# Kernel tuning notes

Measured on AMD Instinct MI355X. Metric: run time of the kernel, lower is better.

## Reference

```python
import jax, jax.numpy as jnp
import numpy as np

N_NODES = 100000
N_EDGES = 1600000
S_FEAT = 16   # static node features
D_FEAT = 8    # dynamic node features
E_FEAT = 4    # edge features
K = 2
EDGE_IN = E_FEAT + 2 * S_FEAT + 2 * D_FEAT  # 52
HIDDEN = 2 * D_FEAT                          # 16


def setup_inputs() -> dict:
    key = jax.random.key(0)
    ks = jax.random.split(key, 12)
    inp = {
        "x_s": jax.random.normal(ks[0], (N_NODES, S_FEAT), jnp.float32),
        "x_d": jax.random.normal(ks[1], (N_NODES, D_FEAT), jnp.float32),
        "edge_attr": jax.random.normal(ks[2], (N_EDGES, E_FEAT), jnp.float32),
        # edge MLP: Linear(EDGE_IN->HIDDEN) + ReLU + Linear(HIDDEN->D_FEAT)
        "W1": jax.random.normal(ks[3], (HIDDEN, EDGE_IN), jnp.float32) / np.sqrt(EDGE_IN),
        "b1": jnp.zeros((HIDDEN,), jnp.float32),
        "W2": jax.random.normal(ks[4], (D_FEAT, HIDDEN), jnp.float32) / np.sqrt(HIDDEN),
        "b2": jnp.zeros((D_FEAT,), jnp.float32),
        # K+1 = 3 filter matrices, Linear(D->D, bias=False): y = x @ W.T
        "Wf0": jax.random.normal(ks[5], (D_FEAT, D_FEAT), jnp.float32) / np.sqrt(D_FEAT),
        "Wf1": jax.random.normal(ks[6], (D_FEAT, D_FEAT), jnp.float32) / np.sqrt(D_FEAT),
        "Wf2": jax.random.normal(ks[7], (D_FEAT, D_FEAT), jnp.float32) / np.sqrt(D_FEAT),
        "edge_index": jax.random.randint(ks[8], (2, N_EDGES), 0, N_NODES, jnp.int64
                                         if jax.config.jax_enable_x64 else jnp.int32),
    }
    return inp


def _edge_mlp(e, W1, b1, W2, b2):
    h = jax.nn.relu(e @ W1.T + b1)
    return h @ W2.T + b2


def reference(x_s, x_d, edge_attr, W1, b1, W2, b2, Wf0, Wf1, Wf2, edge_index):
    row, col = edge_index[0], edge_index[1]
    num_nodes = x_d.shape[0]

    # s_ij depends only on static inputs (x_s, x_d, edge_attr), not on `out`,
    # so it is identical across the K steps; compute it once. The per-step
    # boolean edge mask is applied multiplicatively below, which matches the
    # torch masked-gather/scatter exactly (normalization is per-edge).
    e_ij = jnp.concatenate(
        [x_s[row], x_s[col], x_d[row], x_d[col], edge_attr], axis=1)  # [E, 52]
    s_ij = _edge_mlp(e_ij, W1, b1, W2, b2)                            # [E, D]
    nrm = jnp.linalg.norm(s_ij, axis=1, keepdims=True)
    s_ij = jnp.where(nrm > 0, s_ij / jnp.where(nrm > 0, nrm, 1.0), 0.0)

    filters = [Wf0, Wf1, Wf2]
    out = x_d @ filters[0].T
    for k in range(K):
        mask = out.sum(1) != 0                         # [N]
        edge_mask = (mask[row] | mask[col]).astype(out.dtype)  # [E]
        hydraulic_gradient = out[col] - out[row]       # [E, D]
        shift_sum = hydraulic_gradient * s_ij * edge_mask[:, None]
        scattered = jax.ops.segment_sum(shift_sum, col, num_segments=num_nodes)
        scattered = scattered @ filters[k + 1].T
        out = out + scattered
    return out
```

## Files before the change

### kernel.cpp

```cpp
#include <hip/hip_runtime.h>
#include <hip/hip_fp16.h>

#define S_FEAT 16
#define D_FEAT 8
#define E_FEAT 4
#define EDGE_IN 52
#define HIDDEN 16
#define SCAN_CHUNK 2048
#define NSUB 8

typedef unsigned int uint4v __attribute__((ext_vector_type(4)));
typedef float float4v __attribute__((ext_vector_type(4)));

__device__ __forceinline__ uint4v pack_rec(const float s[8], int row)
{
    int q[8];
#pragma unroll
    for (int i = 0; i < 8; ++i) {
        float v = fminf(fmaxf(s[i] * 2047.f, -2047.f), 2047.f);
        q[i] = (int)rintf(v) & 0xFFF;
    }
    uint4v r;
    r[0] = (unsigned)(q[0] | (q[1] << 12) | (q[2] << 24));
    r[1] = (unsigned)((q[2] >> 8) | (q[3] << 4) | (q[4] << 16) | (q[5] << 28));
    r[2] = (unsigned)((q[5] >> 4) | (q[6] << 8) | (q[7] << 20));
    r[3] = (unsigned)row;
    return r;
}

__device__ __forceinline__ float rec_s(uint4v r, int f)
{
    int off = f * 12;
    unsigned lo = off < 32 ? r[0] : (off < 64 ? r[1] : r[2]);
    unsigned hi = off < 32 ? r[1] : (off < 64 ? r[2] : 0u);
    unsigned sh = (unsigned)off & 31u;
    unsigned long long both = ((unsigned long long)hi << 32) | lo;
    int q = ((int)((unsigned)(both >> sh) << 20)) >> 20;
    return (float)q * (1.f / 2047.f);
}

__device__ __forceinline__ void unpack8h(uint4v w, float* dst)
{
#pragma unroll
    for (int i = 0; i < 4; ++i) {
        unsigned u = w[i];
        __half2 h = *reinterpret_cast<__half2*>(&u);
        float2 f = __half22float2(h);
        dst[2 * i] = f.x; dst[2 * i + 1] = f.y;
    }
}

__device__ __forceinline__ void proj_node(
    int n, const float* __restrict__ x_s, const float* __restrict__ x_d,
    const float* __restrict__ W1, const float* __restrict__ b1,
    const float* __restrict__ Wf0,
    __half* __restrict__ PRh, __half* __restrict__ PCh, float* __restrict__ out)
{
    float xs[S_FEAT], xd[D_FEAT];
    {
        const float4* p = (const float4*)(x_s + (size_t)n * S_FEAT);
#pragma unroll
        for (int q = 0; q < 4; ++q) {
            float4 v = p[q];
            xs[q * 4 + 0] = v.x; xs[q * 4 + 1] = v.y;
            xs[q * 4 + 2] = v.z; xs[q * 4 + 3] = v.w;
        }
        const float4* pd = (const float4*)(x_d + (size_t)n * D_FEAT);
        float4 a = pd[0], b = pd[1];
        xd[0] = a.x; xd[1] = a.y; xd[2] = a.z; xd[3] = a.w;
        xd[4] = b.x; xd[5] = b.y; xd[6] = b.z; xd[7] = b.w;
    }
    __half prh[HIDDEN], pch[HIDDEN];
#pragma unroll
    for (int i = 0; i < HIDDEN; ++i) {
        const float* w = W1 + i * EDGE_IN;
        float a = b1[i], c = 0.f;
#pragma unroll
        for (int j = 0; j < S_FEAT; ++j) {
            a = fmaf(xs[j], w[j], a);
            c = fmaf(xs[j], w[16 + j], c);
        }
#pragma unroll
        for (int j = 0; j < D_FEAT; ++j) {
            a = fmaf(xd[j], w[32 + j], a);
            c = fmaf(xd[j], w[40 + j], c);
        }
        prh[i] = __float2half_rn(a);
        pch[i] = __float2half_rn(c);
    }
    {
        uint4v* pr = (uint4v*)(PRh + (size_t)n * HIDDEN);
        uint4v* pc = (uint4v*)(PCh + (size_t)n * HIDDEN);
        pr[0] = *(uint4v*)&prh[0]; pr[1] = *(uint4v*)&prh[8];
        pc[0] = *(uint4v*)&pch[0]; pc[1] = *(uint4v*)&pch[8];
    }
    float o[D_FEAT];
#pragma unroll
    for (int i = 0; i < D_FEAT; ++i) {
        float acc = 0.f;
#pragma unroll
        for (int j = 0; j < D_FEAT; ++j)
            acc = fmaf(xd[j], Wf0[i * D_FEAT + j], acc);
        o[i] = acc;
    }
    float4* op = (float4*)(out + (size_t)n * D_FEAT);
    op[0] = make_float4(o[0], o[1], o[2], o[3]);
    op[1] = make_float4(o[4], o[5], o[6], o[7]);
}

__device__ __forceinline__ void edge_work(
    const __half* __restrict__ PRh, const __half* __restrict__ PCh,
    const float* __restrict__ edge_attr,
    const float* __restrict__ W1,
    const float* __restrict__ W2, const float* __restrict__ b2,
    int row, int col, int e,
    int* __restrict__ cursor, uint4v* __restrict__ recs)
{
    float pr[HIDDEN], pc[HIDDEN];
    {
        const uint4v* p = (const uint4v*)(PRh + (size_t)row * HIDDEN);
        const uint4v* c = (const uint4v*)(PCh + (size_t)col * HIDDEN);
        uint4v p0 = p[0], p1 = p[1], c0 = c[0], c1 = c[1];
        unpack8h(p0, pr); unpack8h(p1, pr + 8);
        unpack8h(c0, pc); unpack8h(c1, pc + 8);
    }
    float4v ea = __builtin_nontemporal_load(
        (const float4v*)(edge_attr + (size_t)e * E_FEAT));

    float h[HIDDEN];
#pragma unroll
    for (int i = 0; i < HIDDEN; ++i) {
        const float* w = W1 + i * EDGE_IN + 48;
        float acc = pr[i] + pc[i];
        acc = fmaf(ea[0], w[0], acc);
        acc = fmaf(ea[1], w[1], acc);
        acc = fmaf(ea[2], w[2], acc);
        acc = fmaf(ea[3], w[3], acc);
        h[i] = acc > 0.f ? acc : 0.f;
    }

    float s[D_FEAT];
    float nrm2 = 0.f;
#pragma unroll
    for (int i = 0; i < D_FEAT; ++i) {
        float acc = b2[i];
#pragma unroll
        for (int j = 0; j < HIDDEN; ++j)
            acc = fmaf(h[j], W2[i * HIDDEN + j], acc);
        s[i] = acc;
        nrm2 = fmaf(acc, acc, nrm2);
    }
    float nrm = sqrtf(nrm2);
    float inv = nrm > 0.f ? 1.f / nrm : 0.f;
#pragma unroll
    for (int i = 0; i < D_FEAT; ++i) s[i] *= inv;

    uint4v rec = pack_rec(s, row);
    int pos = atomicAdd(&cursor[col], 1);
    __builtin_nontemporal_store(rec, recs + pos);
}

__global__ __launch_bounds__(256) void hist_kernel(
    const int* __restrict__ ei, int E, int N, int* __restrict__ counts8)
{
    int e = blockIdx.x * blockDim.x + threadIdx.x;
    if (e >= E) return;
    int col = __builtin_nontemporal_load(ei + E + e);
    atomicAdd(&counts8[(threadIdx.x & (NSUB - 1)) * N + col], 1);
}

__global__ __launch_bounds__(256) void scan_local_kernel(
    const int* __restrict__ counts8, int* __restrict__ partial,
    int* __restrict__ bsums, int* __restrict__ done, int N, int NB)
{
    __shared__ int sh[256];
    __shared__ int amLast;
    int b = blockIdx.x, t = threadIdx.x;
    int base = b * SCAN_CHUNK + t * 8;
    int v[8];
    int run = 0;
#pragma unroll
    for (int j = 0; j < 8; ++j) {
        int c = 0;
        if (base + j < N) {
#pragma unroll
            for (int s8 = 0; s8 < NSUB; ++s8)
                c += counts8[s8 * N + base + j];
        }
        v[j] = run;
        run += c;
    }
    sh[t] = run;
    __syncthreads();
#pragma unroll
    for (int st = 1; st < 256; st <<= 1) {
        int x = (t >= st) ? sh[t - st] : 0;
        __syncthreads();
        sh[t] += x;
        __syncthreads();
    }
    int excl = sh[t] - run;
#pragma unroll
    for (int j = 0; j < 8; ++j)
        if (base + j < N) partial[base + j] = excl + v[j];

    if (t == 255) atomicExch(&bsums[b], sh[255]);
    __threadfence();
    if (t == 0) amLast = (atomicAdd(done, 1) == NB - 1);
    __syncthreads();
    if (amLast && t < 64) {
        int lane = t;
        int carry = 0;
        for (int cb = 0; cb < NB; cb += 64) {
            int i = cb + lane;
            int orig = (i < NB) ? atomicAdd(&bsums[i], 0) : 0;
            int x = orig;
#pragma unroll
            for (int st = 1; st < 64; st <<= 1) {
                int y = __shfl_up(x, st);
                if (lane >= st) x += y;
            }
            if (i < NB) atomicExch(&bsums[i], carry + x - orig);
            carry += __shfl(x, 63);
        }
    }
}

__global__ __launch_bounds__(256) void proj_scan_kernel(
    int* __restrict__ offsets, int* __restrict__ cursor,
    const int* __restrict__ blocksums,
    const float* __restrict__ x_s, const float* __restrict__ x_d,
    const float* __restrict__ W1, const float* __restrict__ b1,
    const float* __restrict__ Wf0,
    __half* __restrict__ PRh, __half* __restrict__ PCh,
    float* __restrict__ out, int N, int E)
{
    int n = blockIdx.x * blockDim.x + threadIdx.x;
    if (n > N) return;
    if (n == N) { offsets[N] = E; return; }
    int off2 = offsets[n] + blocksums[n / SCAN_CHUNK];
    offsets[n] = off2;
    cursor[n]  = off2;
    proj_node(n, x_s, x_d, W1, b1, Wf0, PRh, PCh, out);
}

__global__ __launch_bounds__(256) void mlp_scatter_proj_kernel(
    const __half* __restrict__ PRh, const __half* __restrict__ PCh,
    const float* __restrict__ edge_attr,
    const float* __restrict__ W1,
    const float* __restrict__ W2, const float* __restrict__ b2,
    const int* __restrict__ ei, int E,
    int* __restrict__ cursor, uint4v* __restrict__ recs)
{
    int e = blockIdx.x * blockDim.x + threadIdx.x;
    if (e >= E) return;
    int row = __builtin_nontemporal_load(ei + e);
    int col = __builtin_nontemporal_load(ei + E + e);
    edge_work(PRh, PCh, edge_attr, W1, W2, b2, row, col, e, cursor, recs);
}

__global__ __launch_bounds__(256) void csr_step_kernel(
    const float* __restrict__ out_in, float* __restrict__ out_out,
    const int* __restrict__ offsets, const uint4v* __restrict__ recs,
    const float* __restrict__ Wf, int N)
{
    int lane = threadIdx.x & 63;
    int node = blockIdx.x * 4 + (threadIdx.x >> 6);
    if (node >= N) return;
    int e_sub = lane >> 3, f = lane & 7;
    int beg = offsets[node], end = offsets[node + 1];
    float outc = out_in[(size_t)node * 8 + f];
    float sc = outc;
    sc += __shfl_xor(sc, 1); sc += __shfl_xor(sc, 2); sc += __shfl_xor(sc, 4);
    bool mc = (sc != 0.f);
    float acc = 0.f;
    for (int base = beg; base < end; base += 8) {
        int e = base + e_sub;
        bool valid = e < end;
        uint4v rec = (uint4v)(0u);
        if (valid) rec = __builtin_nontemporal_load(recs + e);
        int row = (int)rec[3];
        float s = rec_s(rec, f);
        float outr = out_in[(size_t)row * 8 + f];
        float sr = outr;
        sr += __shfl_xor(sr, 1); sr += __shfl_xor(sr, 2); sr += __shfl_xor(sr, 4);
        acc += (mc || sr != 0.f) ? (outc - outr) * s : 0.f;
    }
    acc += __shfl_xor(acc, 8);
    acc += __shfl_xor(acc, 16);
    acc += __shfl_xor(acc, 32);
    float upd = 0.f;
#pragma unroll
    for (int j = 0; j < 8; ++j) {
        float aj = __shfl(acc, (lane & ~7) | j);
        upd = fmaf(Wf[f * 8 + j], aj, upd);
    }
    if (e_sub == 0)
        out_out[(size_t)node * 8 + f] = outc + upd;
}

__device__ __forceinline__ void mlp_sij(
    const float* __restrict__ x_s, const float* __restrict__ x_d,
    const float* __restrict__ edge_attr,
    const float* __restrict__ W1, const float* __restrict__ b1,
    const float* __restrict__ W2, const float* __restrict__ b2,
    int row, int col, int e, float s[D_FEAT])
{
    float in[EDGE_IN];
    {
        const float4* p = (const float4*)(x_s + (size_t)row * S_FEAT);
#pragma unroll
        for (int q = 0; q < 4; ++q) {
            float4 v = p[q];
            in[q * 4 + 0] = v.x; in[q * 4 + 1] = v.y;
            in[q * 4 + 2] = v.z; in[q * 4 + 3] = v.w;
        }
    }
    {
        const float4* p = (const float4*)(x_s + (size_t)col * S_FEAT);
#pragma unroll
        for (int q = 0; q < 4; ++q) {
            float4 v = p[q];
            in[16 + q * 4 + 0] = v.x; in[16 + q * 4 + 1] = v.y;
            in[16 + q * 4 + 2] = v.z; in[16 + q * 4 + 3] = v.w;
        }
    }
    {
        const float4* p = (const float4*)(x_d + (size_t)row * D_FEAT);
#pragma unroll
        for (int q = 0; q < 2; ++q) {
            float4 v = p[q];
            in[32 + q * 4 + 0] = v.x; in[32 + q * 4 + 1] = v.y;
            in[32 + q * 4 + 2] = v.z; in[32 + q * 4 + 3] = v.w;
        }
    }
    {
        const float4* p = (const float4*)(x_d + (size_t)col * D_FEAT);
#pragma unroll
        for (int q = 0; q < 2; ++q) {
            float4 v = p[q];
            in[40 + q * 4 + 0] = v.x; in[40 + q * 4 + 1] = v.y;
            in[40 + q * 4 + 2] = v.z; in[40 + q * 4 + 3] = v.w;
        }
    }
    {
        float4 v = *(const float4*)(edge_attr + (size_t)e * E_FEAT);
        in[48] = v.x; in[49] = v.y; in[50] = v.z; in[51] = v.w;
    }
    float h[HIDDEN];
#pragma unroll
    for (int i = 0; i < HIDDEN; ++i) {
        float acc = b1[i];
#pragma unroll
        for (int j = 0; j < EDGE_IN; ++j)
            acc = fmaf(in[j], W1[i * EDGE_IN + j], acc);
        h[i] = acc > 0.f ? acc : 0.f;
    }
    float nrm2 = 0.f;
#pragma unroll
    for (int i = 0; i < D_FEAT; ++i) {
        float acc = b2[i];
#pragma unroll
        for (int j = 0; j < HIDDEN; ++j)
            acc = fmaf(h[j], W2[i * HIDDEN + j], acc);
        s[i] = acc;
        nrm2 = fmaf(acc, acc, nrm2);
    }
    float nrm = sqrtf(nrm2);
    float inv = nrm > 0.f ? 1.f / nrm : 0.f;
#pragma unroll
    for (int i = 0; i < D_FEAT; ++i) s[i] *= inv;
}

__global__ __launch_bounds__(256) void scan_add_kernel(
    int* __restrict__ offsets, int* __restrict__ cursor,
    const int* __restrict__ blocksums, int N, int E)
{
    int i = blockIdx.x * blockDim.x + threadIdx.x;
    if (i < N) {
        int off2 = offsets[i] + blocksums[i / SCAN_CHUNK];
        offsets[i] = off2;
        cursor[i]  = off2;
    } else if (i == N) {
        offsets[N] = E;
    }
}

__global__ __launch_bounds__(256) void node_init_kernel(
    const float* __restrict__ x_d, const float* __restrict__ Wf0,
    float* __restrict__ out, int N)
{
    int n = blockIdx.x * blockDim.x + threadIdx.x;
    if (n >= N) return;
    float xd[D_FEAT];
    const float4* p = (const float4*)(x_d + (size_t)n * D_FEAT);
    float4 a = p[0], b = p[1];
    xd[0] = a.x; xd[1] = a.y; xd[2] = a.z; xd[3] = a.w;
    xd[4] = b.x; xd[5] = b.y; xd[6] = b.z; xd[7] = b.w;
    float o[D_FEAT];
#pragma unroll
    for (int i = 0; i < D_FEAT; ++i) {
        float acc = 0.f;
#pragma unroll
        for (int j = 0; j < D_FEAT; ++j)
            acc = fmaf(xd[j], Wf0[i * D_FEAT + j], acc);
        o[i] = acc;
    }
    float4* op = (float4*)(out + (size_t)n * D_FEAT);
    op[0] = make_float4(o[0], o[1], o[2], o[3]);
    op[1] = make_float4(o[4], o[5], o[6], o[7]);
}

__global__ __launch_bounds__(256) void mlp_scatter_direct_kernel(
    const float* __restrict__ x_s, const float* __restrict__ x_d,
    const float* __restrict__ edge_attr,
    const float* __restrict__ W1, const float* __restrict__ b1,
    const float* __restrict__ W2, const float* __restrict__ b2,
    const int* __restrict__ ei, int E,
    int* __restrict__ cursor, uint4v* __restrict__ recs)
{
    int e = blockIdx.x * blockDim.x + threadIdx.x;
    if (e >= E) return;
    int row = ei[e], col = ei[E + e];
    float s[D_FEAT];
    mlp_sij(x_s, x_d, edge_attr, W1, b1, W2, b2, row, col, e, s);
    uint4v rec = pack_rec(s, row);
    int pos = atomicAdd(&cursor[col], 1);
    __builtin_nontemporal_store(rec, recs + pos);
}

__global__ __launch_bounds__(256) void fb_node_init_kernel(
    const float* __restrict__ x_d, const float* __restrict__ Wf0,
    float* __restrict__ out, float* __restrict__ scattered, int N)
{
    int n = blockIdx.x * blockDim.x + threadIdx.x;
    if (n >= N) return;
    float xd[D_FEAT];
    const float4* p = (const float4*)(x_d + (size_t)n * D_FEAT);
    float4 a = p[0], b = p[1];
    xd[0] = a.x; xd[1] = a.y; xd[2] = a.z; xd[3] = a.w;
    xd[4] = b.x; xd[5] = b.y; xd[6] = b.z; xd[7] = b.w;
    float o[D_FEAT];
#pragma unroll
    for (int i = 0; i < D_FEAT; ++i) {
        float acc = 0.f;
#pragma unroll
        for (int j = 0; j < D_FEAT; ++j)
            acc = fmaf(xd[j], Wf0[i * D_FEAT + j], acc);
        o[i] = acc;
    }
    float4* op = (float4*)(out + (size_t)n * D_FEAT);
    op[0] = make_float4(o[0], o[1], o[2], o[3]);
    op[1] = make_float4(o[4], o[5], o[6], o[7]);
    float4* sp = (float4*)(scattered + (size_t)n * D_FEAT);
    sp[0] = make_float4(0.f, 0.f, 0.f, 0.f);
    sp[1] = make_float4(0.f, 0.f, 0.f, 0.f);
}

__global__ __launch_bounds__(256) void fb_edge_step_kernel(
    const float* __restrict__ x_s, const float* __restrict__ x_d,
    const float* __restrict__ edge_attr,
    const float* __restrict__ W1, const float* __restrict__ b1,
    const float* __restrict__ W2, const float* __restrict__ b2,
    const float* __restrict__ out,
    const int* __restrict__ ei, int E, float* __restrict__ scattered)
{
    int e = blockIdx.x * blockDim.x + threadIdx.x;
    if (e >= E) return;
    int row = ei[e], col = ei[E + e];
    const float4* pr = (const float4*)(out + (size_t)row * D_FEAT);
    const float4* pc = (const float4*)(out + (size_t)col * D_FEAT);
    float4 r0 = pr[0], r1 = pr[1], c0 = pc[0], c1 = pc[1];
    float srow = r0.x + r0.y + r0.z + r0.w + r1.x + r1.y + r1.z + r1.w;
    float scol = c0.x + c0.y + c0.z + c0.w + c1.x + c1.y + c1.z + c1.w;
    if (srow == 0.f && scol == 0.f) return;
    float s[D_FEAT];
    mlp_sij(x_s, x_d, edge_attr, W1, b1, W2, b2, row, col, e, s);
    float* dst = scattered + (size_t)col * D_FEAT;
    atomicAdd(dst + 0, (c0.x - r0.x) * s[0]);
    atomicAdd(dst + 1, (c0.y - r0.y) * s[1]);
    atomicAdd(dst + 2, (c0.z - r0.z) * s[2]);
    atomicAdd(dst + 3, (c0.w - r0.w) * s[3]);
    atomicAdd(dst + 4, (c1.x - r1.x) * s[4]);
    atomicAdd(dst + 5, (c1.y - r1.y) * s[5]);
    atomicAdd(dst + 6, (c1.z - r1.z) * s[6]);
    atomicAdd(dst + 7, (c1.w - r1.w) * s[7]);
}

__global__ __launch_bounds__(256) void fb_node_update_kernel(
    float* __restrict__ out, float* __restrict__ scattered,
    const float* __restrict__ Wf, int N)
{
    int n = blockIdx.x * blockDim.x + threadIdx.x;
    if (n >= N) return;
    float sc[D_FEAT];
    float4* sp = (float4*)(scattered + (size_t)n * D_FEAT);
    float4 a = sp[0], b = sp[1];
    sc[0] = a.x; sc[1] = a.y; sc[2] = a.z; sc[3] = a.w;
    sc[4] = b.x; sc[5] = b.y; sc[6] = b.z; sc[7] = b.w;
    sp[0] = make_float4(0.f, 0.f, 0.f, 0.f);
    sp[1] = make_float4(0.f, 0.f, 0.f, 0.f);
    float4* op = (float4*)(out + (size_t)n * D_FEAT);
    float4 o0 = op[0], o1 = op[1];
    float o[D_FEAT] = {o0.x, o0.y, o0.z, o0.w, o1.x, o1.y, o1.z, o1.w};
#pragma unroll
    for (int i = 0; i < D_FEAT; ++i) {
        float acc = 0.f;
#pragma unroll
        for (int j = 0; j < D_FEAT; ++j)
            acc = fmaf(sc[j], Wf[i * D_FEAT + j], acc);
        o[i] += acc;
    }
    op[0] = make_float4(o[0], o[1], o[2], o[3]);
    op[1] = make_float4(o[4], o[5], o[6], o[7]);
}

extern "C" void kernel_launch(void* const* d_in, const int* in_sizes, int n_in,
                              void* d_out, int out_size, void* d_ws, size_t ws_size,
                              hipStream_t stream) {
    const float* x_s       = (const float*)d_in[0];
    const float* x_d       = (const float*)d_in[1];
    const float* edge_attr = (const float*)d_in[2];
    const float* W1        = (const float*)d_in[3];
    const float* b1        = (const float*)d_in[4];
    const float* W2        = (const float*)d_in[5];
    const float* b2        = (const float*)d_in[6];
    const float* Wf0       = (const float*)d_in[7];
    const float* Wf1       = (const float*)d_in[8];
    const float* Wf2       = (const float*)d_in[9];
    const int*   ei        = (const int*)d_in[10];

    int N = in_sizes[1] / D_FEAT;
    int E = in_sizes[10] / 2;

    float* out = (float*)d_out;

    size_t off = 0;
    auto carve = [&](size_t bytes) { size_t p = off; off = (off + bytes + 255) & ~255ULL; return p; };
    size_t o_counts  = carve((size_t)NSUB * N * 4);
    size_t o_done    = carve(4);
    const size_t zero_len = off;
    size_t o_offsets = carve((size_t)(N + 1) * 4);
    size_t o_cursor  = carve((size_t)(N + 1) * 4);
    size_t o_bsums   = carve(256 * 4);
    size_t o_bufA    = carve((size_t)N * D_FEAT * 4);
    size_t o_recs    = carve((size_t)E * 16);
    const size_t need_base = off;
    size_t o_PR      = carve((size_t)N * HIDDEN * 2);
    size_t o_PC      = carve((size_t)N * HIDDEN * 2);
    const size_t need_full = off;

    dim3 blk(256);
    dim3 gE((E + 255) / 256);
    dim3 gN((N + 255) / 256);

    if (ws_size >= need_base) {
        char* ws = (char*)d_ws;
        int*   counts8 = (int*)(ws + o_counts);
        int*   done    = (int*)(ws + o_done);
        int*   offsets = (int*)(ws + o_offsets);
        int*   cursor  = (int*)(ws + o_cursor);
        int*   bsums   = (int*)(ws + o_bsums);
        float* bufA    = (float*)(ws + o_bufA);
        uint4v* recs   = (uint4v*)(ws + o_recs);

        const int NB = (N + SCAN_CHUNK - 1) / SCAN_CHUNK;

        hipMemsetAsync(ws, 0, zero_len, stream);
        hist_kernel<<<gE, blk, 0, stream>>>(ei, E, N, counts8);
        scan_local_kernel<<<dim3(NB), blk, 0, stream>>>(
            counts8, offsets, bsums, done, N, NB);

        if (ws_size >= need_full) {
            __half* PRh = (__half*)(ws + o_PR);
            __half* PCh = (__half*)(ws + o_PC);
            proj_scan_kernel<<<dim3((N + 256) / 256), blk, 0, stream>>>(
                offsets, cursor, bsums, x_s, x_d, W1, b1, Wf0, PRh, PCh, out, N, E);
            mlp_scatter_proj_kernel<<<gE, blk, 0, stream>>>(
                PRh, PCh, edge_attr, W1, W2, b2, ei, E, cursor, recs);
        } else {
            scan_add_kernel<<<dim3((N + 256) / 256), blk, 0, stream>>>(
                offsets, cursor, bsums, N, E);
            node_init_kernel<<<gN, blk, 0, stream>>>(x_d, Wf0, out, N);
            mlp_scatter_direct_kernel<<<gE, blk, 0, stream>>>(
                x_s, x_d, edge_attr, W1, b1, W2, b2, ei, E, cursor, recs);
        }

        dim3 gC((N + 3) / 4);
        csr_step_kernel<<<gC, blk, 0, stream>>>(out, bufA, offsets, recs, Wf1, N);
        csr_step_kernel<<<gC, blk, 0, stream>>>(bufA, out, offsets, recs, Wf2, N);
    } else {
        float* scattered = (float*)d_ws;
        fb_node_init_kernel<<<gN, blk, 0, stream>>>(x_d, Wf0, out, scattered, N);
        for (int k = 0; k < 2; ++k) {
            const float* Wfk = (k == 0) ? Wf1 : Wf2;
            fb_edge_step_kernel<<<gE, blk, 0, stream>>>(
                x_s, x_d, edge_attr, W1, b1, W2, b2, out, ei, E, scattered);
            fb_node_update_kernel<<<gN, blk, 0, stream>>>(out, scattered, Wfk, N);
        }
    }
}
```

Baseline: 372.8 us.

## Fuse histogram with node projection, unroll CSR gather, hoist cursor atomic

Moves the per-node projection (PR/PC halves and initial out) out of the scan-add kernel and into the histogram kernel. That kernel now has each thread process four column indices with a vectorized load. The scan-add becomes a tiny separate kernel. The CSR step loop processes two records per lane per iteration to raise memory-level parallelism. The cursor atomic is issued before the MLP so its latency overlaps with the compute. The kernel count is unchanged, but the histogram kernel now carries heavier per-node work, and the extra register pressure in the step loop may reduce occupancy.

```diff
diff --git a/kernel.cpp b/kernel.cpp
--- a/kernel.cpp
+++ b/kernel.cpp
@@ -11,6 +11,7 @@
 
 typedef unsigned int uint4v __attribute__((ext_vector_type(4)));
 typedef float float4v __attribute__((ext_vector_type(4)));
+typedef int int4v __attribute__((ext_vector_type(4)));
 
 __device__ __forceinline__ uint4v pack_rec(const float s[8], int row)
 {
@@ -113,8 +114,7 @@
     const float* __restrict__ edge_attr,
     const float* __restrict__ W1,
     const float* __restrict__ W2, const float* __restrict__ b2,
-    int row, int col, int e,
-    int* __restrict__ cursor, uint4v* __restrict__ recs)
+    int row, int col, int e, int pos, uint4v* __restrict__ recs)
 {
     float pr[HIDDEN], pc[HIDDEN];
     {
@@ -156,8 +156,32 @@
     for (int i = 0; i < D_FEAT; ++i) s[i] *= inv;
 
     uint4v rec = pack_rec(s, row);
-    int pos = atomicAdd(&cursor[col], 1);
     __builtin_nontemporal_store(rec, recs + pos);
+}
+
+__global__ __launch_bounds__(256) void hist_proj_kernel(
+    const int* __restrict__ ei, int E, int N, int* __restrict__ counts8,
+    const float* __restrict__ x_s, const float* __restrict__ x_d,
+    const float* __restrict__ W1, const float* __restrict__ b1,
+    const float* __restrict__ Wf0,
+    __half* __restrict__ PRh, __half* __restrict__ PCh,
+    float* __restrict__ out)
+{
+    int tid = blockIdx.x * blockDim.x + threadIdx.x;
+    int sub = (threadIdx.x & (NSUB - 1)) * N;
+    int e0 = tid * 4;
+    if (e0 + 3 < E) {
+        int4v c = __builtin_nontemporal_load((const int4v*)(ei + E + e0));
+        atomicAdd(&counts8[sub + c[0]], 1);
+        atomicAdd(&counts8[sub + c[1]], 1);
+        atomicAdd(&counts8[sub + c[2]], 1);
+        atomicAdd(&counts8[sub + c[3]], 1);
+    } else {
+        for (int e = e0; e < E; ++e)
+            atomicAdd(&counts8[sub + ei[E + e]], 1);
+    }
+    if (tid < N)
+        proj_node(tid, x_s, x_d, W1, b1, Wf0, PRh, PCh, out);
 }
 
 __global__ __launch_bounds__(256) void hist_kernel(
@@ -226,22 +250,18 @@
     }
 }
 
-__global__ __launch_bounds__(256) void proj_scan_kernel(
+__global__ __launch_bounds__(256) void scan_add_kernel(
     int* __restrict__ offsets, int* __restrict__ cursor,
-    const int* __restrict__ blocksums,
-    const float* __restrict__ x_s, const float* __restrict__ x_d,
-    const float* __restrict__ W1, const float* __restrict__ b1,
-    const float* __restrict__ Wf0,
-    __half* __restrict__ PRh, __half* __restrict__ PCh,
-    float* __restrict__ out, int N, int E)
-{
-    int n = blockIdx.x * blockDim.x + threadIdx.x;
-    if (n > N) return;
-    if (n == N) { offsets[N] = E; return; }
-    int off2 = offsets[n] + blocksums[n / SCAN_CHUNK];
-    offsets[n] = off2;
-    cursor[n]  = off2;
-    proj_node(n, x_s, x_d, W1, b1, Wf0, PRh, PCh, out);
+    const int* __restrict__ blocksums, int N, int E)
+{
+    int i = blockIdx.x * blockDim.x + threadIdx.x;
+    if (i < N) {
+        int off2 = offsets[i] + blocksums[i / SCAN_CHUNK];
+        offsets[i] = off2;
+        cursor[i]  = off2;
+    } else if (i == N) {
+        offsets[N] = E;
+    }
 }
 
 __global__ __launch_bounds__(256) void mlp_scatter_proj_kernel(
@@ -256,7 +276,8 @@
     if (e >= E) return;
     int row = __builtin_nontemporal_load(ei + e);
     int col = __builtin_nontemporal_load(ei + E + e);
-    edge_work(PRh, PCh, edge_attr, W1, W2, b2, row, col, e, cursor, recs);
+    int pos = atomicAdd(&cursor[col], 1);
+    edge_work(PRh, PCh, edge_attr, W1, W2, b2, row, col, e, pos, recs);
 }
 
 __global__ __launch_bounds__(256) void csr_step_kernel(
@@ -274,17 +295,22 @@
     sc += __shfl_xor(sc, 1); sc += __shfl_xor(sc, 2); sc += __shfl_xor(sc, 4);
     bool mc = (sc != 0.f);
     float acc = 0.f;
-    for (int base = beg; base < end; base += 8) {
-        int e = base + e_sub;
-        bool valid = e < end;
-        uint4v rec = (uint4v)(0u);
-        if (valid) rec = __builtin_nontemporal_load(recs + e);
-        int row = (int)rec[3];
-        float s = rec_s(rec, f);
-        float outr = out_in[(size_t)row * 8 + f];
-        float sr = outr;
-        sr += __shfl_xor(sr, 1); sr += __shfl_xor(sr, 2); sr += __shfl_xor(sr, 4);
-        acc += (mc || sr != 0.f) ? (outc - outr) * s : 0.f;
+    for (int base = beg; base < end; base += 16) {
+        int e0 = base + e_sub;
+        int e1 = base + 8 + e_sub;
+        uint4v r0 = (uint4v)(0u), r1 = (uint4v)(0u);
+        if (e0 < end) r0 = __builtin_nontemporal_load(recs + e0);
+        if (e1 < end) r1 = __builtin_nontemporal_load(recs + e1);
+        int row0 = (int)r0[3], row1 = (int)r1[3];
+        float g0 = out_in[(size_t)row0 * 8 + f];
+        float g1 = out_in[(size_t)row1 * 8 + f];
+        float s0 = rec_s(r0, f), s1 = rec_s(r1, f);
+        float sr0 = g0;
+        sr0 += __shfl_xor(sr0, 1); sr0 += __shfl_xor(sr0, 2); sr0 += __shfl_xor(sr0, 4);
+        float sr1 = g1;
+        sr1 += __shfl_xor(sr1, 1); sr1 += __shfl_xor(sr1, 2); sr1 += __shfl_xor(sr1, 4);
+        acc += (mc || sr0 != 0.f) ? (outc - g0) * s0 : 0.f;
+        acc += (mc || sr1 != 0.f) ? (outc - g1) * s1 : 0.f;
     }
     acc += __shfl_xor(acc, 8);
     acc += __shfl_xor(acc, 16);
@@ -370,20 +396,6 @@
     float inv = nrm > 0.f ? 1.f / nrm : 0.f;
 #pragma unroll
     for (int i = 0; i < D_FEAT; ++i) s[i] *= inv;
-}
-
-__global__ __launch_bounds__(256) void scan_add_kernel(
-    int* __restrict__ offsets, int* __restrict__ cursor,
-    const int* __restrict__ blocksums, int N, int E)
-{
-    int i = blockIdx.x * blockDim.x + threadIdx.x;
-    if (i < N) {
-        int off2 = offsets[i] + blocksums[i / SCAN_CHUNK];
-        offsets[i] = off2;
-        cursor[i]  = off2;
-    } else if (i == N) {
-        offsets[N] = E;
-    }
 }
 
 __global__ __launch_bounds__(256) void node_init_kernel(
@@ -422,10 +434,10 @@
     int e = blockIdx.x * blockDim.x + threadIdx.x;
     if (e >= E) return;
     int row = ei[e], col = ei[E + e];
+    int pos = atomicAdd(&cursor[col], 1);
     float s[D_FEAT];
     mlp_sij(x_s, x_d, edge_attr, W1, b1, W2, b2, row, col, e, s);
     uint4v rec = pack_rec(s, row);
-    int pos = atomicAdd(&cursor[col], 1);
     __builtin_nontemporal_store(rec, recs + pos);
 }
 
@@ -567,18 +579,24 @@
         const int NB = (N + SCAN_CHUNK - 1) / SCAN_CHUNK;
 
         hipMemsetAsync(ws, 0, zero_len, stream);
-        hist_kernel<<<gE, blk, 0, stream>>>(ei, E, N, counts8);
-        scan_local_kernel<<<dim3(NB), blk, 0, stream>>>(
-            counts8, offsets, bsums, done, N, NB);
 
         if (ws_size >= need_full) {
             __half* PRh = (__half*)(ws + o_PR);
             __half* PCh = (__half*)(ws + o_PC);
-            proj_scan_kernel<<<dim3((N + 256) / 256), blk, 0, stream>>>(
-                offsets, cursor, bsums, x_s, x_d, W1, b1, Wf0, PRh, PCh, out, N, E);
+            int nth = (E + 3) / 4;
+            if (nth < N) nth = N;
+            hist_proj_kernel<<<dim3((nth + 255) / 256), blk, 0, stream>>>(
+                ei, E, N, counts8, x_s, x_d, W1, b1, Wf0, PRh, PCh, out);
+            scan_local_kernel<<<dim3(NB), blk, 0, stream>>>(
+                counts8, offsets, bsums, done, N, NB);
+            scan_add_kernel<<<dim3((N + 256) / 256), blk, 0, stream>>>(
+                offsets, cursor, bsums, N, E);
             mlp_scatter_proj_kernel<<<gE, blk, 0, stream>>>(
                 PRh, PCh, edge_attr, W1, W2, b2, ei, E, cursor, recs);
         } else {
+            hist_kernel<<<gE, blk, 0, stream>>>(ei, E, N, counts8);
+            scan_local_kernel<<<dim3(NB), blk, 0, stream>>>(
+                counts8, offsets, bsums, done, N, NB);
             scan_add_kernel<<<dim3((N + 256) / 256), blk, 0, stream>>>(
                 offsets, cursor, bsums, N, E);
             node_init_kernel<<<gN, blk, 0, stream>>>(x_d, Wf0, out, N);
```

Measured after the change: 367.9 us. Within noise of the previous version (-1.3%).
